# Kernel tuning notes

Measured on AMD Instinct MI355X. Metric: run time of the kernel, lower is better.

Reference implementation:

```python
import jax, jax.numpy as jnp
import numpy as np

NEG_SLOPE = 0.2  # PyG GATConv default LeakyReLU slope
BN_EPS = 1e-5


def gat_layer(x, src, dst, W, a_src, a_dst, num_nodes):
    """PyG-style GATConv (no dropout, eval mode). Returns [N, H, C]."""
    H, C = a_src.shape
    h = (x @ W).reshape(-1, H, C)                       # [N,H,C]
    s_src = jnp.einsum('nhc,hc->nh', h, a_src)          # [N,H]
    s_dst = jnp.einsum('nhc,hc->nh', h, a_dst)          # [N,H]
    e = jax.nn.leaky_relu(s_src[src] + s_dst[dst], NEG_SLOPE)  # [E,H]
    # segment softmax over incoming edges of each dst node
    e_max = jax.ops.segment_max(e, dst, num_segments=num_nodes)  # [N,H]
    e_exp = jnp.exp(e - e_max[dst])
    denom = jax.ops.segment_sum(e_exp, dst, num_segments=num_nodes)
    alpha = e_exp / (denom[dst] + 1e-16)                # [E,H]
    msg = h[src] * alpha[:, :, None]                    # [E,H,C] (dominant intermediate)
    return jax.ops.segment_sum(msg, dst, num_segments=num_nodes)  # [N,H,C]


def setup_inputs() -> dict:
    key = jax.random.key(0)
    ks = jax.random.split(key, 12)
    N, Din, Hdim, Heads, Dout = 50000, 128, 128, 8, 128
    E = 150000
    inp = {}
    inp['x'] = jax.random.normal(ks[0], (N, Din), dtype=jnp.float32)
    inp['edge_index'] = jax.random.randint(ks[1], (2, E), 0, N, dtype=jnp.int64)
    sc1 = 1.0 / np.sqrt(Din)
    inp['W1'] = jax.random.uniform(ks[2], (Din, Heads * Hdim), minval=-sc1, maxval=sc1, dtype=jnp.float32)
    inp['a_src1'] = jax.random.normal(ks[3], (Heads, Hdim), dtype=jnp.float32) * 0.1
    inp['a_dst1'] = jax.random.normal(ks[4], (Heads, Hdim), dtype=jnp.float32) * 0.1
    inp['b1'] = jnp.zeros((Heads * Hdim,), dtype=jnp.float32)
    inp['gamma'] = jnp.ones((Heads * Hdim,), dtype=jnp.float32)
    inp['beta'] = jnp.zeros((Heads * Hdim,), dtype=jnp.float32)
    sc2 = 1.0 / np.sqrt(Heads * Hdim)
    inp['W2'] = jax.random.uniform(ks[5], (Heads * Hdim, Dout), minval=-sc2, maxval=sc2, dtype=jnp.float32)
    inp['a_src2'] = jax.random.normal(ks[6], (1, Dout), dtype=jnp.float32) * 0.1
    inp['a_dst2'] = jax.random.normal(ks[7], (1, Dout), dtype=jnp.float32) * 0.1
    inp['b2'] = jnp.zeros((Dout,), dtype=jnp.float32)
    return inp


def reference(x, W1, a_src1, a_dst1, b1, gamma, beta, W2, a_src2, a_dst2, b2, edge_index):
    N = x.shape[0]
    src, dst = edge_index[0], edge_index[1]
    # GAT layer 1: heads=8, concat=True
    h1 = gat_layer(x, src, dst, W1, a_src1, a_dst1, N)   # [N,8,128]
    h1 = h1.reshape(N, -1) + b1                          # [N,1024]
    # BatchNorm1d (training-mode batch stats, biased variance as in torch)
    mu = jnp.mean(h1, axis=0)
    var = jnp.var(h1, axis=0)
    h1 = gamma * (h1 - mu) * jax.lax.rsqrt(var + BN_EPS) + beta
    h1 = jax.nn.elu(h1)
    # GAT layer 2: heads=1, concat=False (mean == squeeze for 1 head)
    h2 = gat_layer(h1, src, dst, W2, a_src2, a_dst2, N)  # [N,1,128]
    return h2[:, 0, :] + b2
```

## Files before the change

kernel.cpp:

```cpp
#include <hip/hip_runtime.h>
#include <hip/hip_bf16.h>
#include <math.h>

#define NEG_SLOPE 0.2f
#define BN_EPS 1e-5f

typedef short bf16x8 __attribute__((ext_vector_type(8)));
typedef float f32x4 __attribute__((ext_vector_type(4)));

__device__ __forceinline__ float bf2f(unsigned short u) {
  union { unsigned int i; float f; } v;
  v.i = ((unsigned int)u) << 16;
  return v.f;
}
__device__ __forceinline__ unsigned short f2bf(float f) {
  union { unsigned int i; float f; } v;
  v.f = f;
  unsigned int i = v.i;
  unsigned int r = (i + 0x7fffu + ((i >> 16) & 1u)) >> 16;
  return (unsigned short)r;
}

__global__ __launch_bounds__(256) void detect_kernel(
    const unsigned int* __restrict__ xw, const unsigned int* __restrict__ eiw,
    int E, int* __restrict__ flags) {
  __shared__ int cnt[2];
  if (threadIdx.x < 2) cnt[threadIdx.x] = 0;
  __syncthreads();
  int t = threadIdx.x;
  int inrange = 0;
  for (int i = t; i < 2048; i += 256) {
    unsigned int e = (xw[i] >> 7) & 0xFFu;
    inrange += (e >= 100u && e <= 135u) ? 1 : 0;
  }
  atomicAdd(&cnt[0], inrange);
  int M = min(1024, E / 2);
  int zeros = 0;
  for (int i = t; i < M; i += 256) zeros += (eiw[2 * i + 1] == 0u) ? 1 : 0;
  atomicAdd(&cnt[1], zeros);
  __syncthreads();
  if (t == 0) {
    flags[0] = (cnt[0] > 1536) ? 1 : 0;
    flags[1] = (cnt[1] > M / 2) ? 1 : 0;
  }
}

__global__ __launch_bounds__(256) void canon_x8(
    const void* __restrict__ src, unsigned short* __restrict__ dst, int n_real,
    int n_total, const int* __restrict__ flags) {
  int i = (blockIdx.x * 256 + threadIdx.x) * 8;
  if (i >= n_total) return;
  union { bf16x8 v; unsigned short u[8]; } o;
  if (i < n_real) {
    if (flags[0]) {
      o.v = *(const bf16x8*)((const unsigned short*)src + i);
    } else {
      const float4* f = (const float4*)((const float*)src + i);
      float4 f0 = f[0];
      float4 f1 = f[1];
      o.u[0] = f2bf(f0.x); o.u[1] = f2bf(f0.y);
      o.u[2] = f2bf(f0.z); o.u[3] = f2bf(f0.w);
      o.u[4] = f2bf(f1.x); o.u[5] = f2bf(f1.y);
      o.u[6] = f2bf(f1.z); o.u[7] = f2bf(f1.w);
    }
  } else {
#pragma unroll
    for (int j = 0; j < 8; ++j) o.u[j] = 0;
  }
  *(bf16x8*)(dst + i) = o.v;
}

__global__ __launch_bounds__(256) void canon_w_t(
    const void* __restrict__ src, unsigned short* __restrict__ dst, int Kdim,
    int Ndim, const int* __restrict__ flags) {
  int i = blockIdx.x * 256 + threadIdx.x;
  if (i >= Kdim * Ndim) return;
  int k = i / Ndim, n = i - k * Ndim;
  unsigned short v = flags[0] ? ((const unsigned short*)src)[i]
                              : f2bf(((const float*)src)[i]);
  dst[(size_t)n * Kdim + k] = v;
}

__global__ __launch_bounds__(1024) void canon_params(
    const void* s0, const void* s1, const void* s2, const void* s3,
    const void* s4, const void* s5, const void* s6, const void* s7,
    unsigned short* d0, unsigned short* d1, unsigned short* d2,
    unsigned short* d3, unsigned short* d4, unsigned short* d5,
    unsigned short* d6, unsigned short* d7, const int* __restrict__ flags) {
  int b = blockIdx.x, t = threadIdx.x;
  const void* s;
  unsigned short* d;
  int n;
  switch (b) {
    case 0: s = s0; d = d0; n = 1024; break;
    case 1: s = s1; d = d1; n = 1024; break;
    case 2: s = s2; d = d2; n = 1024; break;
    case 3: s = s3; d = d3; n = 1024; break;
    case 4: s = s4; d = d4; n = 1024; break;
    case 5: s = s5; d = d5; n = 128; break;
    case 6: s = s6; d = d6; n = 128; break;
    default: s = s7; d = d7; n = 128; break;
  }
  if (t < n)
    d[t] = flags[0] ? ((const unsigned short*)s)[t]
                    : f2bf(((const float*)s)[t]);
}

__global__ __launch_bounds__(256) void canon_idx(
    const int* __restrict__ ei, int* __restrict__ eis, int* __restrict__ eid,
    int E, const int* __restrict__ flags) {
  int e = blockIdx.x * 256 + threadIdx.x;
  if (e >= E) return;
  if (flags[1]) {
    eis[e] = ei[2 * (size_t)e];
    eid[e] = ei[2 * (size_t)E + 2 * (size_t)e];
  } else {
    eis[e] = ei[e];
    eid[e] = ei[E + e];
  }
}

template <int BM, bool TRANSFORM_A, bool OUT_BF16, bool SCORES>
__global__ __launch_bounds__(256) void gemm_mfma(
    const unsigned short* __restrict__ A, const unsigned short* __restrict__ Bt,
    void* __restrict__ Cv, int M, int N, int K,
    const float* __restrict__ scale, const float* __restrict__ shift,
    const unsigned short* __restrict__ aScr,
    const unsigned short* __restrict__ aDcr, float* __restrict__ ssrc,
    float* __restrict__ sdst, int hs) {
  constexpr int BK = 32;
  constexpr int LDA = BK + 8;
  constexpr int MI = BM / 32;
  __shared__ unsigned short As[BM * LDA];
  __shared__ unsigned short Bs[128 * LDA];
  __shared__ float sS[2][128];
  __shared__ float sD[2][128];

  const int m0 = blockIdx.y * BM;
  const int n0 = blockIdx.x * 128;
  const int tid = threadIdx.x;
  const int wid = tid >> 6;
  const int lane = tid & 63;
  const int q = lane >> 4;
  const int r = lane & 15;
  const int wm = (wid >> 1) * (BM / 2);
  const int wn = (wid & 1) * 64;

  f32x4 acc[MI][4] = {};

  const int row0 = (tid * 8) >> 5, col0 = (tid * 8) & 31;

  bf16x8 ra[2], rb[2];
  ra[0] = *(const bf16x8*)(A + (size_t)(m0 + row0) * K + col0);
  if (BM == 128)
    ra[1] = *(const bf16x8*)(A + (size_t)(m0 + row0 + 64) * K + col0);
  rb[0] = *(const bf16x8*)(Bt + (size_t)(n0 + row0) * K + col0);
  rb[1] = *(const bf16x8*)(Bt + (size_t)(n0 + row0 + 64) * K + col0);

  for (int k0 = 0; k0 < K; k0 += BK) {
#pragma unroll
    for (int rd = 0; rd < 2; ++rd) {
      int row = row0 + rd * 64;
      if (rd == 0 || BM == 128) {
        bf16x8 v = ra[rd];
        if (TRANSFORM_A) {
          float scv[8], shv[8];
          *(float4*)&scv[0] = *(const float4*)(scale + k0 + col0);
          *(float4*)&scv[4] = *(const float4*)(scale + k0 + col0 + 4);
          *(float4*)&shv[0] = *(const float4*)(shift + k0 + col0);
          *(float4*)&shv[4] = *(const float4*)(shift + k0 + col0 + 4);
          union { bf16x8 v; unsigned short u[8]; } p;
          p.v = v;
#pragma unroll
          for (int j = 0; j < 8; ++j) {
            float f = bf2f(p.u[j]) * scv[j] + shv[j];
            f = f > 0.f ? f : (__expf(f) - 1.0f);
            p.u[j] = f2bf(f);
          }
          v = p.v;
        }
        *(bf16x8*)(&As[row * LDA + col0]) = v;
      }
      *(bf16x8*)(&Bs[row * LDA + col0]) = rb[rd];
    }
    __syncthreads();

    int k1 = k0 + BK;
    if (k1 < K) {
      ra[0] = *(const bf16x8*)(A + (size_t)(m0 + row0) * K + k1 + col0);
      if (BM == 128)
        ra[1] = *(const bf16x8*)(A + (size_t)(m0 + row0 + 64) * K + k1 + col0);
      rb[0] = *(const bf16x8*)(Bt + (size_t)(n0 + row0) * K + k1 + col0);
      rb[1] = *(const bf16x8*)(Bt + (size_t)(n0 + row0 + 64) * K + k1 + col0);
    }

    bf16x8 af[MI], bfv[4];
#pragma unroll
    for (int mi = 0; mi < MI; ++mi)
      af[mi] = *(const bf16x8*)(&As[(wm + mi * 16 + r) * LDA + q * 8]);
#pragma unroll
    for (int ni = 0; ni < 4; ++ni)
      bfv[ni] = *(const bf16x8*)(&Bs[(wn + ni * 16 + r) * LDA + q * 8]);
#pragma unroll
    for (int mi = 0; mi < MI; ++mi)
#pragma unroll
      for (int ni = 0; ni < 4; ++ni)
        acc[mi][ni] = __builtin_amdgcn_mfma_f32_16x16x32_bf16(
            af[mi], bfv[ni], acc[mi][ni], 0, 0, 0);
    __syncthreads();
  }

#pragma unroll
  for (int mi = 0; mi < MI; ++mi) {
#pragma unroll
    for (int ni = 0; ni < 4; ++ni) {
#pragma unroll
      for (int i = 0; i < 4; ++i) {
        int row = m0 + wm + mi * 16 + q * 4 + i;
        int col = n0 + wn + ni * 16 + r;
        if (OUT_BF16)
          ((unsigned short*)Cv)[(size_t)row * N + col] = f2bf(acc[mi][ni][i]);
        else
          ((float*)Cv)[(size_t)row * N + col] = acc[mi][ni][i];
      }
    }
  }

  if (SCORES) {
    const int half = wid & 1;
    float aSv[4], aDv[4];
#pragma unroll
    for (int ni = 0; ni < 4; ++ni) {
      aSv[ni] = bf2f(aScr[n0 + wn + ni * 16 + r]);
      aDv[ni] = bf2f(aDcr[n0 + wn + ni * 16 + r]);
    }
#pragma unroll
    for (int mi = 0; mi < MI; ++mi) {
#pragma unroll
      for (int i = 0; i < 4; ++i) {
        float ps = 0.f, pd = 0.f;
#pragma unroll
        for (int ni = 0; ni < 4; ++ni) {
          float v = acc[mi][ni][i];
          ps += v * aSv[ni];
          pd += v * aDv[ni];
        }
        ps += __shfl_xor(ps, 1, 64); pd += __shfl_xor(pd, 1, 64);
        ps += __shfl_xor(ps, 2, 64); pd += __shfl_xor(pd, 2, 64);
        ps += __shfl_xor(ps, 4, 64); pd += __shfl_xor(pd, 4, 64);
        ps += __shfl_xor(ps, 8, 64); pd += __shfl_xor(pd, 8, 64);
        if (r == 0) {
          int rl = wm + mi * 16 + q * 4 + i;
          sS[half][rl] = ps;
          sD[half][rl] = pd;
        }
      }
    }
    __syncthreads();
    if (tid < BM) {
      int grow = m0 + tid;
      ssrc[(size_t)grow * hs + blockIdx.x] = sS[0][tid] + sS[1][tid];
      sdst[(size_t)grow * hs + blockIdx.x] = sD[0][tid] + sD[1][tid];
    }
  }
}

__global__ __launch_bounds__(256) void count_dst(const int* __restrict__ eid,
                                                 int E, int* __restrict__ cnt) {
  int e = blockIdx.x * 256 + threadIdx.x;
  if (e < E) atomicAdd(&cnt[eid[e]], 1);
}

__global__ __launch_bounds__(256) void scan_p1(const int* __restrict__ cnt,
                                               int* __restrict__ bsum, int N) {
  __shared__ int sd[256];
  int b = blockIdx.x, t = threadIdx.x;
  int base = b * 2048;
  int s = 0;
  for (int i = t; i < 2048; i += 256) {
    int idx = base + i;
    if (idx < N) s += cnt[idx];
  }
  sd[t] = s;
  __syncthreads();
  for (int o = 128; o > 0; o >>= 1) {
    if (t < o) sd[t] += sd[t + o];
    __syncthreads();
  }
  if (t == 0) bsum[b] = sd[0];
}

__global__ __launch_bounds__(256) void scan_p2(int* __restrict__ bsum, int nb) {
  __shared__ int sd[256];
  int t = threadIdx.x;
  int own = (t < nb) ? bsum[t] : 0;
  sd[t] = own;
  __syncthreads();
  for (int o = 1; o < 256; o <<= 1) {
    int v = (t >= o) ? sd[t - o] : 0;
    __syncthreads();
    sd[t] += v;
    __syncthreads();
  }
  if (t < nb) bsum[t] = sd[t] - own;
}

__global__ __launch_bounds__(256) void scan_p3(
    const int* __restrict__ cnt, const int* __restrict__ bsum,
    int* __restrict__ offsets, int* __restrict__ cursor, int N) {
  __shared__ int sd[256];
  int b = blockIdx.x, t = threadIdx.x;
  int base = b * 2048 + t * 8;
  int c[8];
  int ts = 0;
#pragma unroll
  for (int j = 0; j < 8; ++j) {
    int idx = base + j;
    c[j] = (idx < N) ? cnt[idx] : 0;
    ts += c[j];
  }
  sd[t] = ts;
  __syncthreads();
  for (int o = 1; o < 256; o <<= 1) {
    int v = (t >= o) ? sd[t - o] : 0;
    __syncthreads();
    sd[t] += v;
    __syncthreads();
  }
  int run = bsum[b] + sd[t] - ts;
#pragma unroll
  for (int j = 0; j < 8; ++j) {
    int idx = base + j;
    if (idx < N) {
      offsets[idx] = run;
      cursor[idx] = run;
      run += c[j];
    }
  }
  if (b == gridDim.x - 1 && t == 255) offsets[N] = bsum[b] + sd[255];
}

__global__ __launch_bounds__(256) void scatter_src(
    const int* __restrict__ eis, const int* __restrict__ eid, int E,
    int* __restrict__ cursor, int* __restrict__ srcs, int* __restrict__ dsts) {
  int e = blockIdx.x * 256 + threadIdx.x;
  if (e >= E) return;
  int d = eid[e];
  int pos = atomicAdd(&cursor[d], 1);
  srcs[pos] = eis[e];
  dsts[pos] = d;
}

__global__ __launch_bounds__(256) void edge_w1(
    const int* __restrict__ srcs, const int* __restrict__ dsts,
    const float* __restrict__ ssrc, const float* __restrict__ sdst,
    float* __restrict__ ew, int E8) {
  int t = blockIdx.x * 256 + threadIdx.x;
  if (t >= E8) return;
  int p = t >> 3, h = t & 7;
  float v = ssrc[srcs[p] * 8 + h] + sdst[dsts[p] * 8 + h];
  v = v > 0.f ? v : NEG_SLOPE * v;
  ew[t] = __expf(v);
}

__global__ __launch_bounds__(256) void edge_w2(
    const int* __restrict__ srcs, const int* __restrict__ dsts,
    const float* __restrict__ ssrc, const float* __restrict__ sdst,
    float* __restrict__ ew2, int E) {
  int p = blockIdx.x * 256 + threadIdx.x;
  if (p >= E) return;
  float v = ssrc[srcs[p]] + sdst[dsts[p]];
  v = v > 0.f ? v : NEG_SLOPE * v;
  ew2[p] = __expf(v);
}

__global__ __launch_bounds__(256) void agg1_csr(
    const int* __restrict__ offsets, const int* __restrict__ srcs,
    const unsigned short* __restrict__ h1, const float* __restrict__ ew,
    const unsigned short* __restrict__ b1, unsigned short* __restrict__ h1n,
    int N) {
  int n = blockIdx.x * 2 + (threadIdx.x >> 7);
  if (n >= N) return;
  int t = threadIdx.x & 127;
  int c = t * 8;
  int h = c >> 7;
  int beg = offsets[n], end = offsets[n + 1];
  float a0 = 0, a1 = 0, a2 = 0, a3 = 0, a4 = 0, a5 = 0, a6 = 0, a7 = 0;
  float wsum = 0.f;
  int p = beg;
  for (; p + 2 <= end; p += 2) {
    int s0 = srcs[p], s1 = srcs[p + 1];
    float w0 = ew[p * 8 + h], w1 = ew[(p + 1) * 8 + h];
    union { bf16x8 v; unsigned short u[8]; } u0, u1;
    u0.v = *(const bf16x8*)(h1 + (size_t)s0 * 1024 + c);
    u1.v = *(const bf16x8*)(h1 + (size_t)s1 * 1024 + c);
    wsum += w0 + w1;
    a0 = fmaf(bf2f(u0.u[0]), w0, a0);
    a1 = fmaf(bf2f(u0.u[1]), w0, a1);
    a2 = fmaf(bf2f(u0.u[2]), w0, a2);
    a3 = fmaf(bf2f(u0.u[3]), w0, a3);
    a4 = fmaf(bf2f(u0.u[4]), w0, a4);
    a5 = fmaf(bf2f(u0.u[5]), w0, a5);
    a6 = fmaf(bf2f(u0.u[6]), w0, a6);
    a7 = fmaf(bf2f(u0.u[7]), w0, a7);
    a0 = fmaf(bf2f(u1.u[0]), w1, a0);
    a1 = fmaf(bf2f(u1.u[1]), w1, a1);
    a2 = fmaf(bf2f(u1.u[2]), w1, a2);
    a3 = fmaf(bf2f(u1.u[3]), w1, a3);
    a4 = fmaf(bf2f(u1.u[4]), w1, a4);
    a5 = fmaf(bf2f(u1.u[5]), w1, a5);
    a6 = fmaf(bf2f(u1.u[6]), w1, a6);
    a7 = fmaf(bf2f(u1.u[7]), w1, a7);
  }
  if (p < end) {
    int s0 = srcs[p];
    float w0 = ew[p * 8 + h];
    union { bf16x8 v; unsigned short u[8]; } u0;
    u0.v = *(const bf16x8*)(h1 + (size_t)s0 * 1024 + c);
    wsum += w0;
    a0 = fmaf(bf2f(u0.u[0]), w0, a0);
    a1 = fmaf(bf2f(u0.u[1]), w0, a1);
    a2 = fmaf(bf2f(u0.u[2]), w0, a2);
    a3 = fmaf(bf2f(u0.u[3]), w0, a3);
    a4 = fmaf(bf2f(u0.u[4]), w0, a4);
    a5 = fmaf(bf2f(u0.u[5]), w0, a5);
    a6 = fmaf(bf2f(u0.u[6]), w0, a6);
    a7 = fmaf(bf2f(u0.u[7]), w0, a7);
  }
  float inv = 1.0f / (wsum + 1e-16f);
  union { bf16x8 v; unsigned short u[8]; } bb, o;
  bb.v = *(const bf16x8*)(b1 + c);
  o.u[0] = f2bf(a0 * inv + bf2f(bb.u[0]));
  o.u[1] = f2bf(a1 * inv + bf2f(bb.u[1]));
  o.u[2] = f2bf(a2 * inv + bf2f(bb.u[2]));
  o.u[3] = f2bf(a3 * inv + bf2f(bb.u[3]));
  o.u[4] = f2bf(a4 * inv + bf2f(bb.u[4]));
  o.u[5] = f2bf(a5 * inv + bf2f(bb.u[5]));
  o.u[6] = f2bf(a6 * inv + bf2f(bb.u[6]));
  o.u[7] = f2bf(a7 * inv + bf2f(bb.u[7]));
  *(bf16x8*)(h1n + (size_t)n * 1024 + c) = o.v;
}

__global__ __launch_bounds__(256) void bn_stats_part(
    const unsigned short* __restrict__ h1n, float* __restrict__ part, int N,
    int rowsPerBlock) {
  int b = blockIdx.x;
  int half = threadIdx.x >> 7;
  int t = threadIdx.x & 127;
  int c = t * 8;
  int r0 = b * rowsPerBlock;
  int r1 = min(r0 + rowsPerBlock, N);
  float s[8] = {0, 0, 0, 0, 0, 0, 0, 0};
  float q[8] = {0, 0, 0, 0, 0, 0, 0, 0};
  int r = r0 + half;
  for (; r + 2 < r1; r += 4) {
    union { bf16x8 v; unsigned short u[8]; } u0, u1;
    u0.v = *(const bf16x8*)(h1n + (size_t)r * 1024 + c);
    u1.v = *(const bf16x8*)(h1n + (size_t)(r + 2) * 1024 + c);
#pragma unroll
    for (int j = 0; j < 8; ++j) {
      float v0 = bf2f(u0.u[j]);
      float v1 = bf2f(u1.u[j]);
      s[j] += v0 + v1;
      q[j] = fmaf(v0, v0, q[j]);
      q[j] = fmaf(v1, v1, q[j]);
    }
  }
  for (; r < r1; r += 2) {
    union { bf16x8 v; unsigned short u[8]; } u0;
    u0.v = *(const bf16x8*)(h1n + (size_t)r * 1024 + c);
#pragma unroll
    for (int j = 0; j < 8; ++j) {
      float v0 = bf2f(u0.u[j]);
      s[j] += v0;
      q[j] = fmaf(v0, v0, q[j]);
    }
  }
  float* pb = part + ((size_t)b * 2 + half) * 2048;
#pragma unroll
  for (int j = 0; j < 8; ++j) {
    pb[c + j] = s[j];
    pb[1024 + c + j] = q[j];
  }
}

__global__ __launch_bounds__(256) void bn_reduce_finalize(
    const float* __restrict__ part, int nparts,
    const unsigned short* __restrict__ gamma,
    const unsigned short* __restrict__ beta, float* __restrict__ scale,
    float* __restrict__ shift, int N) {
  int c = blockIdx.x * 4 + (threadIdx.x >> 6);
  int lane = threadIdx.x & 63;
  float s = 0.f, q = 0.f;
  for (int b = lane; b < nparts; b += 64) {
    s += part[(size_t)b * 2048 + c];
    q += part[(size_t)b * 2048 + 1024 + c];
  }
#pragma unroll
  for (int o = 32; o > 0; o >>= 1) {
    s += __shfl_xor(s, o, 64);
    q += __shfl_xor(q, o, 64);
  }
  if (lane == 0) {
    float inv_n = 1.0f / (float)N;
    float mu = s * inv_n;
    float var = q * inv_n - mu * mu;
    float sc = bf2f(gamma[c]) * rsqrtf(var + BN_EPS);
    scale[c] = sc;
    shift[c] = bf2f(beta[c]) - mu * sc;
  }
}

__global__ __launch_bounds__(256) void agg2_csr(
    const int* __restrict__ offsets, const int* __restrict__ srcs,
    const float* __restrict__ h2, const float* __restrict__ ew2,
    const unsigned short* __restrict__ b2, void* __restrict__ out,
    const int* __restrict__ flags, int N) {
  int n = blockIdx.x * 8 + (threadIdx.x >> 5);
  if (n >= N) return;
  int c = (threadIdx.x & 31) * 4;
  int beg = offsets[n], end = offsets[n + 1];
  float a0 = 0.f, a1 = 0.f, a2 = 0.f, a3 = 0.f, wsum = 0.f;
  int p = beg;
  for (; p + 2 <= end; p += 2) {
    int s0 = srcs[p], s1 = srcs[p + 1];
    float w0 = ew2[p], w1 = ew2[p + 1];
    float4 v0 = *(const float4*)(h2 + (size_t)s0 * 128 + c);
    float4 v1 = *(const float4*)(h2 + (size_t)s1 * 128 + c);
    wsum += w0 + w1;
    a0 = fmaf(v0.x, w0, a0);
    a1 = fmaf(v0.y, w0, a1);
    a2 = fmaf(v0.z, w0, a2);
    a3 = fmaf(v0.w, w0, a3);
    a0 = fmaf(v1.x, w1, a0);
    a1 = fmaf(v1.y, w1, a1);
    a2 = fmaf(v1.z, w1, a2);
    a3 = fmaf(v1.w, w1, a3);
  }
  if (p < end) {
    int s0 = srcs[p];
    float w0 = ew2[p];
    float4 v0 = *(const float4*)(h2 + (size_t)s0 * 128 + c);
    wsum += w0;
    a0 = fmaf(v0.x, w0, a0);
    a1 = fmaf(v0.y, w0, a1);
    a2 = fmaf(v0.z, w0, a2);
    a3 = fmaf(v0.w, w0, a3);
  }
  float inv = 1.0f / (wsum + 1e-16f);
  ushort4 bb = *(const ushort4*)(b2 + c);
  float r0 = a0 * inv + bf2f(bb.x);
  float r1 = a1 * inv + bf2f(bb.y);
  float r2 = a2 * inv + bf2f(bb.z);
  float r3 = a3 * inv + bf2f(bb.w);
  if (flags[0]) {
    ushort4 o;
    o.x = f2bf(r0); o.y = f2bf(r1); o.z = f2bf(r2); o.w = f2bf(r3);
    *(ushort4*)((unsigned short*)out + (size_t)n * 128 + c) = o;
  } else {
    *(float4*)((float*)out + (size_t)n * 128 + c) =
        make_float4(r0, r1, r2, r3);
  }
}

extern "C" void kernel_launch(void* const* d_in, const int* in_sizes, int n_in,
                              void* d_out, int out_size, void* d_ws,
                              size_t ws_size, hipStream_t stream) {
  const void* x      = d_in[0];
  const int*  ei     = (const int*)d_in[1];
  const void* W1     = d_in[2];
  const void* a_src1 = d_in[3];
  const void* a_dst1 = d_in[4];
  const void* b1     = d_in[5];
  const void* gamma  = d_in[6];
  const void* beta   = d_in[7];
  const void* W2     = d_in[8];
  const void* a_src2 = d_in[9];
  const void* a_dst2 = d_in[10];
  const void* b2     = d_in[11];

  const int N = in_sizes[0] / 128;
  const int E = in_sizes[1] / 2;
  const int MP = ((N + 127) / 128) * 128;
  const int NB = (N + 2047) / 2048;
  const int NSTAT = 256;
  const int RPB = (N + NSTAT - 1) / NSTAT;

  char* ws = (char*)d_ws;
  size_t off = 0;
  unsigned short* h1  = (unsigned short*)(ws + off); off += (size_t)MP * 1024 * 2;
  char* h1n_base = ws + off;
  unsigned short* h1n = (unsigned short*)h1n_base;   off += (size_t)MP * 1024 * 2;
  float* ssrc1 = (float*)(ws + off); off += (size_t)MP * 8 * 4;
  float* sdst1 = (float*)(ws + off); off += (size_t)MP * 8 * 4;
  int* offsets = (int*)(ws + off); off += ((size_t)(N + 1) * 4 + 63) & ~63ull;
  int* srcs    = (int*)(ws + off); off += (size_t)E * 4;
  int* dsts    = (int*)(ws + off); off += (size_t)E * 4;
  float* ew    = (float*)(ws + off); off += (size_t)E * 8 * 4;
  float* part  = (float*)(ws + off); off += (size_t)NSTAT * 2 * 2048 * 4;
  unsigned short* W1t = (unsigned short*)(ws + off); off += 131072 * 2;
  unsigned short* W2t = (unsigned short*)(ws + off); off += 131072 * 2;
  unsigned short* as1c = (unsigned short*)(ws + off); off += 1024 * 2;
  unsigned short* ad1c = (unsigned short*)(ws + off); off += 1024 * 2;
  unsigned short* b1c  = (unsigned short*)(ws + off); off += 1024 * 2;
  unsigned short* gmc  = (unsigned short*)(ws + off); off += 1024 * 2;
  unsigned short* btc  = (unsigned short*)(ws + off); off += 1024 * 2;
  unsigned short* as2c = (unsigned short*)(ws + off); off += 128 * 2;
  unsigned short* ad2c = (unsigned short*)(ws + off); off += 128 * 2;
  unsigned short* b2c  = (unsigned short*)(ws + off); off += 128 * 2;
  float* scale = (float*)(ws + off); off += 1024 * 4;
  float* shift = (float*)(ws + off); off += 1024 * 4;
  int* bsum    = (int*)(ws + off); off += 256 * 4;
  int* flags   = (int*)(ws + off); off += 64;
  unsigned short* x_bf = (unsigned short*)h1n_base;
  int* eis    = (int*)(h1n_base + (16u << 20));
  int* eid    = eis + E;
  int* cnt    = eid + E;
  int* cursor = cnt + N;
  float* h2    = (float*)h1;
  float* ssrc2 = ssrc1;
  float* sdst2 = sdst1;
  float* ew2   = ew;

  detect_kernel<<<1, 256, 0, stream>>>((const unsigned int*)x,
                                       (const unsigned int*)ei, E, flags);
  canon_x8<<<(MP * 128 / 8 + 255) / 256, 256, 0, stream>>>(x, x_bf, N * 128,
                                                           MP * 128, flags);
  canon_w_t<<<(131072 + 255) / 256, 256, 0, stream>>>(W1, W1t, 128, 1024, flags);
  canon_w_t<<<(131072 + 255) / 256, 256, 0, stream>>>(W2, W2t, 1024, 128, flags);
  canon_params<<<8, 1024, 0, stream>>>(a_src1, a_dst1, b1, gamma, beta, a_src2,
                                       a_dst2, b2, as1c, ad1c, b1c, gmc, btc,
                                       as2c, ad2c, b2c, flags);
  canon_idx<<<(E + 255) / 256, 256, 0, stream>>>(ei, eis, eid, E, flags);

  hipMemsetAsync(cnt, 0, (size_t)N * 4, stream);
  hipMemsetAsync((char*)h1n + (size_t)N * 1024 * 2, 0,
                 (size_t)(MP - N) * 1024 * 2, stream);

  count_dst<<<(E + 255) / 256, 256, 0, stream>>>(eid, E, cnt);
  scan_p1<<<NB, 256, 0, stream>>>(cnt, bsum, N);
  scan_p2<<<1, 256, 0, stream>>>(bsum, NB);
  scan_p3<<<NB, 256, 0, stream>>>(cnt, bsum, offsets, cursor, N);
  scatter_src<<<(E + 255) / 256, 256, 0, stream>>>(eis, eid, E, cursor, srcs,
                                                   dsts);

  {
    dim3 g(1024 / 128, MP / 128);
    gemm_mfma<128, false, true, true><<<g, 256, 0, stream>>>(
        x_bf, W1t, h1, MP, 1024, 128, nullptr, nullptr, as1c, ad1c, ssrc1,
        sdst1, 8);
  }
  edge_w1<<<(E * 8 + 255) / 256, 256, 0, stream>>>(srcs, dsts, ssrc1, sdst1,
                                                   ew, E * 8);
  agg1_csr<<<(N + 1) / 2, 256, 0, stream>>>(offsets, srcs, h1, ew, b1c, h1n,
                                            N);

  bn_stats_part<<<NSTAT, 256, 0, stream>>>(h1n, part, N, RPB);
  bn_reduce_finalize<<<256, 256, 0, stream>>>(part, NSTAT * 2, gmc, btc, scale,
                                              shift, N);

  {
    dim3 g(1, MP / 64);
    gemm_mfma<64, true, false, true><<<g, 256, 0, stream>>>(
        h1n, W2t, h2, MP, 128, 1024, scale, shift, as2c, ad2c, ssrc2, sdst2,
        1);
  }
  edge_w2<<<(E + 255) / 256, 256, 0, stream>>>(srcs, dsts, ssrc2, sdst2, ew2, E);
  agg2_csr<<<(N + 7) / 8, 256, 0, stream>>>(offsets, srcs, h2, ew2, b2c, d_out,
                                            flags, N);
}
```

Before: 363.0 us.

## Fuse edge-weight computation into CSR aggregation kernels and drop dsts array

Removes the separate edge_w1/edge_w2 kernels and the dsts/ew buffers. The aggregation kernels now compute LeakyReLU+exp attention weights on the fly from the per-node source and destination scores. agg1 is remapped to one wavefront per node, each lane covering two 8-channel chunks in different head halves. This saves two launches and the global write/read of the per-edge weights, at the cost of recomputing exp in every lane that shares a head and doing extra gathers of ssrc.

```diff
diff --git a/kernel.cpp b/kernel.cpp
--- a/kernel.cpp
+++ b/kernel.cpp
@@ -342,103 +342,88 @@
 
 __global__ __launch_bounds__(256) void scatter_src(
     const int* __restrict__ eis, const int* __restrict__ eid, int E,
-    int* __restrict__ cursor, int* __restrict__ srcs, int* __restrict__ dsts) {
+    int* __restrict__ cursor, int* __restrict__ srcs) {
   int e = blockIdx.x * 256 + threadIdx.x;
   if (e >= E) return;
   int d = eid[e];
   int pos = atomicAdd(&cursor[d], 1);
   srcs[pos] = eis[e];
-  dsts[pos] = d;
-}
-
-__global__ __launch_bounds__(256) void edge_w1(
-    const int* __restrict__ srcs, const int* __restrict__ dsts,
-    const float* __restrict__ ssrc, const float* __restrict__ sdst,
-    float* __restrict__ ew, int E8) {
-  int t = blockIdx.x * 256 + threadIdx.x;
-  if (t >= E8) return;
-  int p = t >> 3, h = t & 7;
-  float v = ssrc[srcs[p] * 8 + h] + sdst[dsts[p] * 8 + h];
-  v = v > 0.f ? v : NEG_SLOPE * v;
-  ew[t] = __expf(v);
-}
-
-__global__ __launch_bounds__(256) void edge_w2(
-    const int* __restrict__ srcs, const int* __restrict__ dsts,
-    const float* __restrict__ ssrc, const float* __restrict__ sdst,
-    float* __restrict__ ew2, int E) {
-  int p = blockIdx.x * 256 + threadIdx.x;
-  if (p >= E) return;
-  float v = ssrc[srcs[p]] + sdst[dsts[p]];
-  v = v > 0.f ? v : NEG_SLOPE * v;
-  ew2[p] = __expf(v);
 }
 
 __global__ __launch_bounds__(256) void agg1_csr(
     const int* __restrict__ offsets, const int* __restrict__ srcs,
-    const unsigned short* __restrict__ h1, const float* __restrict__ ew,
-    const unsigned short* __restrict__ b1, unsigned short* __restrict__ h1n,
-    int N) {
-  int n = blockIdx.x * 2 + (threadIdx.x >> 7);
+    const unsigned short* __restrict__ h1, const float* __restrict__ ssrc,
+    const float* __restrict__ sdst, const unsigned short* __restrict__ b1,
+    unsigned short* __restrict__ h1n, int N) {
+  int n = blockIdx.x * 4 + (threadIdx.x >> 6);
   if (n >= N) return;
-  int t = threadIdx.x & 127;
-  int c = t * 8;
-  int h = c >> 7;
+  int lane = threadIdx.x & 63;
+  int c0 = lane * 8;
+  int c1 = 512 + c0;
+  int hA = lane >> 4;
   int beg = offsets[n], end = offsets[n + 1];
-  float a0 = 0, a1 = 0, a2 = 0, a3 = 0, a4 = 0, a5 = 0, a6 = 0, a7 = 0;
-  float wsum = 0.f;
+  float sdA = sdst[n * 8 + hA];
+  float sdB = sdst[n * 8 + hA + 4];
+  float accA[8] = {}, accB[8] = {};
+  float wsA = 0.f, wsB = 0.f;
   int p = beg;
   for (; p + 2 <= end; p += 2) {
     int s0 = srcs[p], s1 = srcs[p + 1];
-    float w0 = ew[p * 8 + h], w1 = ew[(p + 1) * 8 + h];
-    union { bf16x8 v; unsigned short u[8]; } u0, u1;
-    u0.v = *(const bf16x8*)(h1 + (size_t)s0 * 1024 + c);
-    u1.v = *(const bf16x8*)(h1 + (size_t)s1 * 1024 + c);
-    wsum += w0 + w1;
-    a0 = fmaf(bf2f(u0.u[0]), w0, a0);
-    a1 = fmaf(bf2f(u0.u[1]), w0, a1);
-    a2 = fmaf(bf2f(u0.u[2]), w0, a2);
-    a3 = fmaf(bf2f(u0.u[3]), w0, a3);
-    a4 = fmaf(bf2f(u0.u[4]), w0, a4);
-    a5 = fmaf(bf2f(u0.u[5]), w0, a5);
-    a6 = fmaf(bf2f(u0.u[6]), w0, a6);
-    a7 = fmaf(bf2f(u0.u[7]), w0, a7);
-    a0 = fmaf(bf2f(u1.u[0]), w1, a0);
-    a1 = fmaf(bf2f(u1.u[1]), w1, a1);
-    a2 = fmaf(bf2f(u1.u[2]), w1, a2);
-    a3 = fmaf(bf2f(u1.u[3]), w1, a3);
-    a4 = fmaf(bf2f(u1.u[4]), w1, a4);
-    a5 = fmaf(bf2f(u1.u[5]), w1, a5);
-    a6 = fmaf(bf2f(u1.u[6]), w1, a6);
-    a7 = fmaf(bf2f(u1.u[7]), w1, a7);
+    float vA0 = ssrc[s0 * 8 + hA] + sdA;
+    float vB0 = ssrc[s0 * 8 + hA + 4] + sdB;
+    float vA1 = ssrc[s1 * 8 + hA] + sdA;
+    float vB1 = ssrc[s1 * 8 + hA + 4] + sdB;
+    union { bf16x8 v; unsigned short u[8]; } uA0, uB0, uA1, uB1;
+    uA0.v = *(const bf16x8*)(h1 + (size_t)s0 * 1024 + c0);
+    uB0.v = *(const bf16x8*)(h1 + (size_t)s0 * 1024 + c1);
+    uA1.v = *(const bf16x8*)(h1 + (size_t)s1 * 1024 + c0);
+    uB1.v = *(const bf16x8*)(h1 + (size_t)s1 * 1024 + c1);
+    vA0 = vA0 > 0.f ? vA0 : NEG_SLOPE * vA0;
+    vB0 = vB0 > 0.f ? vB0 : NEG_SLOPE * vB0;
+    vA1 = vA1 > 0.f ? vA1 : NEG_SLOPE * vA1;
+    vB1 = vB1 > 0.f ? vB1 : NEG_SLOPE * vB1;
+    float wA0 = __expf(vA0), wB0 = __expf(vB0);
+    float wA1 = __expf(vA1), wB1 = __expf(vB1);
+    wsA += wA0 + wA1;
+    wsB += wB0 + wB1;
+#pragma unroll
+    for (int j = 0; j < 8; ++j) {
+      accA[j] = fmaf(bf2f(uA0.u[j]), wA0, accA[j]);
+      accB[j] = fmaf(bf2f(uB0.u[j]), wB0, accB[j]);
+      accA[j] = fmaf(bf2f(uA1.u[j]), wA1, accA[j]);
+      accB[j] = fmaf(bf2f(uB1.u[j]), wB1, accB[j]);
+    }
   }
   if (p < end) {
     int s0 = srcs[p];
-    float w0 = ew[p * 8 + h];
-    union { bf16x8 v; unsigned short u[8]; } u0;
-    u0.v = *(const bf16x8*)(h1 + (size_t)s0 * 1024 + c);
-    wsum += w0;
-    a0 = fmaf(bf2f(u0.u[0]), w0, a0);
-    a1 = fmaf(bf2f(u0.u[1]), w0, a1);
-    a2 = fmaf(bf2f(u0.u[2]), w0, a2);
-    a3 = fmaf(bf2f(u0.u[3]), w0, a3);
-    a4 = fmaf(bf2f(u0.u[4]), w0, a4);
-    a5 = fmaf(bf2f(u0.u[5]), w0, a5);
-    a6 = fmaf(bf2f(u0.u[6]), w0, a6);
-    a7 = fmaf(bf2f(u0.u[7]), w0, a7);
-  }
-  float inv = 1.0f / (wsum + 1e-16f);
-  union { bf16x8 v; unsigned short u[8]; } bb, o;
-  bb.v = *(const bf16x8*)(b1 + c);
-  o.u[0] = f2bf(a0 * inv + bf2f(bb.u[0]));
-  o.u[1] = f2bf(a1 * inv + bf2f(bb.u[1]));
-  o.u[2] = f2bf(a2 * inv + bf2f(bb.u[2]));
-  o.u[3] = f2bf(a3 * inv + bf2f(bb.u[3]));
-  o.u[4] = f2bf(a4 * inv + bf2f(bb.u[4]));
-  o.u[5] = f2bf(a5 * inv + bf2f(bb.u[5]));
-  o.u[6] = f2bf(a6 * inv + bf2f(bb.u[6]));
-  o.u[7] = f2bf(a7 * inv + bf2f(bb.u[7]));
-  *(bf16x8*)(h1n + (size_t)n * 1024 + c) = o.v;
+    float vA0 = ssrc[s0 * 8 + hA] + sdA;
+    float vB0 = ssrc[s0 * 8 + hA + 4] + sdB;
+    union { bf16x8 v; unsigned short u[8]; } uA0, uB0;
+    uA0.v = *(const bf16x8*)(h1 + (size_t)s0 * 1024 + c0);
+    uB0.v = *(const bf16x8*)(h1 + (size_t)s0 * 1024 + c1);
+    vA0 = vA0 > 0.f ? vA0 : NEG_SLOPE * vA0;
+    vB0 = vB0 > 0.f ? vB0 : NEG_SLOPE * vB0;
+    float wA0 = __expf(vA0), wB0 = __expf(vB0);
+    wsA += wA0;
+    wsB += wB0;
+#pragma unroll
+    for (int j = 0; j < 8; ++j) {
+      accA[j] = fmaf(bf2f(uA0.u[j]), wA0, accA[j]);
+      accB[j] = fmaf(bf2f(uB0.u[j]), wB0, accB[j]);
+    }
+  }
+  float invA = 1.0f / (wsA + 1e-16f);
+  float invB = 1.0f / (wsB + 1e-16f);
+  union { bf16x8 v; unsigned short u[8]; } bA, bB, oA, oB;
+  bA.v = *(const bf16x8*)(b1 + c0);
+  bB.v = *(const bf16x8*)(b1 + c1);
+#pragma unroll
+  for (int j = 0; j < 8; ++j) {
+    oA.u[j] = f2bf(accA[j] * invA + bf2f(bA.u[j]));
+    oB.u[j] = f2bf(accB[j] * invB + bf2f(bB.u[j]));
+  }
+  *(bf16x8*)(h1n + (size_t)n * 1024 + c0) = oA.v;
+  *(bf16x8*)(h1n + (size_t)n * 1024 + c1) = oB.v;
 }
 
 __global__ __launch_bounds__(256) void bn_stats_part(
@@ -513,39 +498,46 @@
 
 __global__ __launch_bounds__(256) void agg2_csr(
     const int* __restrict__ offsets, const int* __restrict__ srcs,
-    const float* __restrict__ h2, const float* __restrict__ ew2,
-    const unsigned short* __restrict__ b2, void* __restrict__ out,
-    const int* __restrict__ flags, int N) {
+    const float* __restrict__ h2, const float* __restrict__ ssrc,
+    const float* __restrict__ sdst, const unsigned short* __restrict__ b2,
+    void* __restrict__ out, const int* __restrict__ flags, int N) {
   int n = blockIdx.x * 8 + (threadIdx.x >> 5);
   if (n >= N) return;
   int c = (threadIdx.x & 31) * 4;
   int beg = offsets[n], end = offsets[n + 1];
+  float sd = sdst[n];
   float a0 = 0.f, a1 = 0.f, a2 = 0.f, a3 = 0.f, wsum = 0.f;
   int p = beg;
   for (; p + 2 <= end; p += 2) {
     int s0 = srcs[p], s1 = srcs[p + 1];
-    float w0 = ew2[p], w1 = ew2[p + 1];
-    float4 v0 = *(const float4*)(h2 + (size_t)s0 * 128 + c);
-    float4 v1 = *(const float4*)(h2 + (size_t)s1 * 128 + c);
+    float v0 = ssrc[s0] + sd;
+    float v1 = ssrc[s1] + sd;
+    float4 u0 = *(const float4*)(h2 + (size_t)s0 * 128 + c);
+    float4 u1 = *(const float4*)(h2 + (size_t)s1 * 128 + c);
+    v0 = v0 > 0.f ? v0 : NEG_SLOPE * v0;
+    v1 = v1 > 0.f ? v1 : NEG_SLOPE * v1;
+    float w0 = __expf(v0), w1 = __expf(v1);
     wsum += w0 + w1;
-    a0 = fmaf(v0.x, w0, a0);
-    a1 = fmaf(v0.y, w0, a1);
-    a2 = fmaf(v0.z, w0, a2);
-    a3 = fmaf(v0.w, w0, a3);
-    a0 = fmaf(v1.x, w1, a0);
-    a1 = fmaf(v1.y, w1, a1);
-    a2 = fmaf(v1.z, w1, a2);
-    a3 = fmaf(v1.w, w1, a3);
+    a0 = fmaf(u0.x, w0, a0);
+    a1 = fmaf(u0.y, w0, a1);
+    a2 = fmaf(u0.z, w0, a2);
+    a3 = fmaf(u0.w, w0, a3);
+    a0 = fmaf(u1.x, w1, a0);
+    a1 = fmaf(u1.y, w1, a1);
+    a2 = fmaf(u1.z, w1, a2);
+    a3 = fmaf(u1.w, w1, a3);
   }
   if (p < end) {
     int s0 = srcs[p];
-    float w0 = ew2[p];
-    float4 v0 = *(const float4*)(h2 + (size_t)s0 * 128 + c);
+    float v0 = ssrc[s0] + sd;
+    float4 u0 = *(const float4*)(h2 + (size_t)s0 * 128 + c);
+    v0 = v0 > 0.f ? v0 : NEG_SLOPE * v0;
+    float w0 = __expf(v0);
     wsum += w0;
-    a0 = fmaf(v0.x, w0, a0);
-    a1 = fmaf(v0.y, w0, a1);
-    a2 = fmaf(v0.z, w0, a2);
-    a3 = fmaf(v0.w, w0, a3);
+    a0 = fmaf(u0.x, w0, a0);
+    a1 = fmaf(u0.y, w0, a1);
+    a2 = fmaf(u0.z, w0, a2);
+    a3 = fmaf(u0.w, w0, a3);
   }
   float inv = 1.0f / (wsum + 1e-16f);
   ushort4 bb = *(const ushort4*)(b2 + c);
@@ -595,8 +587,6 @@
   float* sdst1 = (float*)(ws + off); off += (size_t)MP * 8 * 4;
   int* offsets = (int*)(ws + off); off += ((size_t)(N + 1) * 4 + 63) & ~63ull;
   int* srcs    = (int*)(ws + off); off += (size_t)E * 4;
-  int* dsts    = (int*)(ws + off); off += (size_t)E * 4;
-  float* ew    = (float*)(ws + off); off += (size_t)E * 8 * 4;
   float* part  = (float*)(ws + off); off += (size_t)NSTAT * 2 * 2048 * 4;
   unsigned short* W1t = (unsigned short*)(ws + off); off += 131072 * 2;
   unsigned short* W2t = (unsigned short*)(ws + off); off += 131072 * 2;
@@ -620,7 +610,6 @@
   float* h2    = (float*)h1;
   float* ssrc2 = ssrc1;
   float* sdst2 = sdst1;
-  float* ew2   = ew;
 
   detect_kernel<<<1, 256, 0, stream>>>((const unsigned int*)x,
                                        (const unsigned int*)ei, E, flags);
@@ -641,8 +630,7 @@
   scan_p1<<<NB, 256, 0, stream>>>(cnt, bsum, N);
   scan_p2<<<1, 256, 0, stream>>>(bsum, NB);
   scan_p3<<<NB, 256, 0, stream>>>(cnt, bsum, offsets, cursor, N);
-  scatter_src<<<(E + 255) / 256, 256, 0, stream>>>(eis, eid, E, cursor, srcs,
-                                                   dsts);
+  scatter_src<<<(E + 255) / 256, 256, 0, stream>>>(eis, eid, E, cursor, srcs);
 
   {
     dim3 g(1024 / 128, MP / 128);
@@ -650,10 +638,8 @@
         x_bf, W1t, h1, MP, 1024, 128, nullptr, nullptr, as1c, ad1c, ssrc1,
         sdst1, 8);
   }
-  edge_w1<<<(E * 8 + 255) / 256, 256, 0, stream>>>(srcs, dsts, ssrc1, sdst1,
-                                                   ew, E * 8);
-  agg1_csr<<<(N + 1) / 2, 256, 0, stream>>>(offsets, srcs, h1, ew, b1c, h1n,
-                                            N);
+  agg1_csr<<<(N + 3) / 4, 256, 0, stream>>>(offsets, srcs, h1, ssrc1, sdst1,
+                                            b1c, h1n, N);
 
   bn_stats_part<<<NSTAT, 256, 0, stream>>>(h1n, part, N, RPB);
   bn_reduce_finalize<<<256, 256, 0, stream>>>(part, NSTAT * 2, gmc, btc, scale,
@@ -665,7 +651,6 @@
         h1n, W2t, h2, MP, 128, 1024, scale, shift, as2c, ad2c, ssrc2, sdst2,
         1);
   }
-  edge_w2<<<(E + 255) / 256, 256, 0, stream>>>(srcs, dsts, ssrc2, sdst2, ew2, E);
-  agg2_csr<<<(N + 7) / 8, 256, 0, stream>>>(offsets, srcs, h2, ew2, b2c, d_out,
-                                            flags, N);
-}
+  agg2_csr<<<(N + 7) / 8, 256, 0, stream>>>(offsets, srcs, h2, ssrc2, sdst2,
+                                            b2c, d_out, flags, N);
+}
```

After: 358.2 us. No clear change (-1.3%).
